# Optimization experiments

Hardware: AMD Instinct MI355X
Metric: run time of the kernel (lower is better)

Reference implementation:

```python
import math
import jax, jax.numpy as jnp
import numpy as np

B, T, E, H = 2, 2048, 1024, 16
HS = E // H  # head size = 64
NEG = jnp.float32(-1e10)


def setup_inputs() -> dict:
    key = jax.random.key(0)
    ks = jax.random.split(key, 7)
    return {
        "query": jax.random.normal(ks[0], (B, T, E), jnp.float32),
        "key": jax.random.normal(ks[1], (B, T, E), jnp.float32),
        "value": jax.random.normal(ks[2], (B, T, E), jnp.float32),
        "Wq": jax.random.normal(ks[3], (E, E), jnp.float32) * 0.02,
        "Wk": jax.random.normal(ks[4], (E, E), jnp.float32) * 0.02,
        "Wv": jax.random.normal(ks[5], (E, E), jnp.float32) * 0.02,
        "Wp": jax.random.normal(ks[6], (E, E), jnp.float32) * 0.02,
    }


def reference(query, key, value, Wq, Wk, Wv, Wp):
    # QKV projections (no bias), split into heads: [B, H, T, HS]
    q = (query @ Wq).reshape(B, T, H, HS).transpose(0, 2, 1, 3)
    k = (key @ Wk).reshape(B, T, H, HS).transpose(0, 2, 1, 3)
    v = (value @ Wv).reshape(B, T, H, HS).transpose(0, 2, 1, 3)
    # scaled dot-product scores [B, H, T, T]
    att = jnp.einsum("bhqd,bhkd->bhqk", q, k) / math.sqrt(HS)
    # additive causal mask (tril allowed)
    causal = jnp.tril(jnp.ones((T, T), dtype=att.dtype))
    att = att + jnp.where(causal == 0, NEG, jnp.float32(0.0))[None, None]
    att = jax.nn.softmax(att, axis=-1)
    # dropout rate 0 / deterministic -> identity
    y = jnp.einsum("bhqk,bhkd->bhqd", att, v)
    y = y.transpose(0, 2, 1, 3).reshape(B, T, E)
    y = y @ Wp
    return y
```

## Files before the change

### kernel.cpp

```cpp
#include <hip/hip_runtime.h>

#define TB 2
#define TT 2048
#define TE 1024
#define TH 16
#define THS 64
#define TM (TB * TT)

typedef __attribute__((ext_vector_type(8))) short short8;
typedef __attribute__((ext_vector_type(4))) float f32x4;
typedef __attribute__((ext_vector_type(16))) float f32x16;

__device__ __forceinline__ f32x4 mfma16(short8 a, short8 b, f32x4 c) {
    return __builtin_amdgcn_mfma_f32_16x16x32_bf16(a, b, c, 0, 0, 0);
}
__device__ __forceinline__ f32x16 mfma32(short8 a, short8 b, f32x16 c) {
    return __builtin_amdgcn_mfma_f32_32x32x16_bf16(a, b, c, 0, 0, 0);
}

__device__ __forceinline__ void gload_lds16(const void* g, void* l) {
    __builtin_amdgcn_global_load_lds(
        (const __attribute__((address_space(1))) void*)g,
        (__attribute__((address_space(3))) void*)l, 16, 0, 0);
}

__device__ __forceinline__ unsigned short f2bf(float f) {
    unsigned int u = __float_as_uint(f);
    u += 0x7fff + ((u >> 16) & 1);
    return (unsigned short)(u >> 16);
}

__device__ __forceinline__ unsigned cvtpk_bf16(float lo, float hi) {
    unsigned r;
    asm("v_cvt_pk_bf16_f32 %0, %1, %2" : "=v"(r) : "v"(lo), "v"(hi));
    return r;
}
__device__ __forceinline__ void plswap(unsigned& a, unsigned& b) {
    asm("v_permlane32_swap_b32 %0, %1" : "+v"(a), "+v"(b));
}

__global__ __launch_bounds__(256) void cast3_f32_bf16(
    const float* __restrict__ a, const float* __restrict__ b,
    const float* __restrict__ c, unsigned short* __restrict__ oa,
    unsigned short* __restrict__ ob, unsigned short* __restrict__ oc, int n4) {
    const float* src = (blockIdx.y == 0) ? a : (blockIdx.y == 1) ? b : c;
    unsigned short* dst = (blockIdx.y == 0) ? oa : (blockIdx.y == 1) ? ob : oc;
    int i = blockIdx.x * 256 + threadIdx.x;
    if (i < n4) {
        float4 v = ((const float4*)src)[i];
        ushort4 o;
        o.x = f2bf(v.x); o.y = f2bf(v.y); o.z = f2bf(v.z); o.w = f2bf(v.w);
        ((ushort4*)dst)[i] = o;
    }
}

__global__ __launch_bounds__(256) void transpose_cast_w4(
    const float* __restrict__ W0, const float* __restrict__ W1,
    const float* __restrict__ W2, const float* __restrict__ W3,
    unsigned short* __restrict__ T0, unsigned short* __restrict__ T1,
    unsigned short* __restrict__ T2, unsigned short* __restrict__ T3) {
    __shared__ float Ts[32][33];
    const int z = blockIdx.z;
    const float* W = (z == 0) ? W0 : (z == 1) ? W1 : (z == 2) ? W2 : W3;
    unsigned short* Wt = (z == 0) ? T0 : (z == 1) ? T1 : (z == 2) ? T2 : T3;
    const int r0 = blockIdx.y * 32, c0 = blockIdx.x * 32;
    const int t = threadIdx.x;
    const int r = t >> 3, c = (t & 7) * 4;
    float4 v = *(const float4*)&W[(size_t)(r0 + r) * TE + c0 + c];
    Ts[r][c] = v.x; Ts[r][c + 1] = v.y; Ts[r][c + 2] = v.z; Ts[r][c + 3] = v.w;
    __syncthreads();
    ushort4 o;
    o.x = f2bf(Ts[c + 0][r]); o.y = f2bf(Ts[c + 1][r]);
    o.z = f2bf(Ts[c + 2][r]); o.w = f2bf(Ts[c + 3][r]);
    *(ushort4*)&Wt[(size_t)(c0 + r) * TE + r0 + c] = o;
}

__global__ __launch_bounds__(512, 2) void gemm_qkv(
    const unsigned short* __restrict__ qc, const unsigned short* __restrict__ kc,
    const unsigned short* __restrict__ vc, const unsigned short* __restrict__ Wqt,
    const unsigned short* __restrict__ Wkt, const unsigned short* __restrict__ Wvt,
    unsigned short* __restrict__ Qb, unsigned short* __restrict__ Kb,
    unsigned short* __restrict__ Vt) {
    __shared__ unsigned short LDS[65536];

    const int z = blockIdx.z;
    const unsigned short* A  = (z == 0) ? qc : (z == 1) ? kc : vc;
    const unsigned short* Bt = (z == 0) ? Wqt : (z == 1) ? Wkt : Wvt;

    const int tid = threadIdx.x;
    const int wv = tid >> 6, lane = tid & 63;
    const int wr = wv >> 2, wc = wv & 3;
    const int quad = lane >> 4, l16 = lane & 15;
    const int bm = blockIdx.x * 256, bn = blockIdx.y * 256;

    const int srow = lane >> 2;
    const int scol = (((lane & 3) ^ ((srow >> 1) & 3))) * 8;
    const int rchunk = (quad ^ ((l16 >> 1) & 3)) * 8;

    f32x4 acc[8][4];
    const f32x4 fz = {0.f, 0.f, 0.f, 0.f};
    #pragma unroll
    for (int i = 0; i < 8; ++i)
        #pragma unroll
        for (int j = 0; j < 4; ++j) acc[i][j] = fz;

    auto stageA = [&](int t, int hi) {
        const int buf = t & 1, k0 = t * 64;
        unsigned short* base = &LDS[buf * 16384];
        #pragma unroll
        for (int j = 0; j < 2; ++j) {
            const int e = wv * 2 + j;
            const int kk = e >> 3, i3 = e & 7;
            const int cr = hi * 4 + (i3 & 3) + ((i3 >> 2) << 3);
            gload_lds16(A + (size_t)(bm + cr * 16 + srow) * TE + k0 + kk * 32 + scol,
                        base + kk * 8192 + cr * 512 + lane * 8);
        }
    };
    auto stageB = [&](int t, int hi) {
        const int buf = t & 1, k0 = t * 64;
        unsigned short* base = &LDS[32768 + buf * 16384];
        #pragma unroll
        for (int j = 0; j < 2; ++j) {
            const int e = wv * 2 + j;
            const int kk = e >> 3, i3 = e & 7;
            const int cc = ((i3 >> 1) << 2) + (i3 & 1) + hi * 2;
            gload_lds16(Bt + (size_t)(bn + cc * 16 + srow) * TE + k0 + kk * 32 + scol,
                        base + kk * 8192 + cc * 512 + lane * 8);
        }
    };

    auto ktile = [&](int t, int buf, bool st, bool predrain) {
        const unsigned short* Al = &LDS[buf * 16384];
        const unsigned short* Bl = &LDS[32768 + buf * 16384];
        short8 af[4][2], blo[2][2], bhi[2][2];
        #pragma unroll
        for (int mi = 0; mi < 4; ++mi)
            #pragma unroll
            for (int kk = 0; kk < 2; ++kk)
                af[mi][kk] = *(const short8*)&Al[kk * 8192 + (wr * 8 + mi) * 512 + l16 * 32 + rchunk];
        #pragma unroll
        for (int nj = 0; nj < 2; ++nj)
            #pragma unroll
            for (int kk = 0; kk < 2; ++kk)
                blo[nj][kk] = *(const short8*)&Bl[kk * 8192 + (wc * 4 + nj) * 512 + l16 * 32 + rchunk];
        __builtin_amdgcn_s_barrier();
        asm volatile("s_waitcnt lgkmcnt(0)" ::: "memory");
        __builtin_amdgcn_sched_barrier(0);
        __builtin_amdgcn_s_setprio(1);
        #pragma unroll
        for (int mi = 0; mi < 4; ++mi)
            #pragma unroll
            for (int nj = 0; nj < 2; ++nj)
                #pragma unroll
                for (int kk = 0; kk < 2; ++kk)
                    acc[mi][nj] = mfma16(af[mi][kk], blo[nj][kk], acc[mi][nj]);
        __builtin_amdgcn_s_setprio(0);
        __builtin_amdgcn_sched_barrier(0);
        __builtin_amdgcn_s_barrier();
        #pragma unroll
        for (int nj = 0; nj < 2; ++nj)
            #pragma unroll
            for (int kk = 0; kk < 2; ++kk)
                bhi[nj][kk] = *(const short8*)&Bl[kk * 8192 + (wc * 4 + 2 + nj) * 512 + l16 * 32 + rchunk];
        if (st) stageA(t + 2, 0);
        __builtin_amdgcn_s_barrier();
        asm volatile("s_waitcnt lgkmcnt(0)" ::: "memory");
        __builtin_amdgcn_sched_barrier(0);
        __builtin_amdgcn_s_setprio(1);
        #pragma unroll
        for (int mi = 0; mi < 4; ++mi)
            #pragma unroll
            for (int nj = 0; nj < 2; ++nj)
                #pragma unroll
                for (int kk = 0; kk < 2; ++kk)
                    acc[mi][2 + nj] = mfma16(af[mi][kk], bhi[nj][kk], acc[mi][2 + nj]);
        __builtin_amdgcn_s_setprio(0);
        __builtin_amdgcn_sched_barrier(0);
        __builtin_amdgcn_s_barrier();
        #pragma unroll
        for (int mi = 0; mi < 4; ++mi)
            #pragma unroll
            for (int kk = 0; kk < 2; ++kk)
                af[mi][kk] = *(const short8*)&Al[kk * 8192 + (wr * 8 + 4 + mi) * 512 + l16 * 32 + rchunk];
        if (st) stageB(t + 2, 0);
        __builtin_amdgcn_s_barrier();
        asm volatile("s_waitcnt lgkmcnt(0)" ::: "memory");
        __builtin_amdgcn_sched_barrier(0);
        __builtin_amdgcn_s_setprio(1);
        #pragma unroll
        for (int mi = 0; mi < 4; ++mi)
            #pragma unroll
            for (int nj = 0; nj < 2; ++nj)
                #pragma unroll
                for (int kk = 0; kk < 2; ++kk)
                    acc[4 + mi][nj] = mfma16(af[mi][kk], blo[nj][kk], acc[4 + mi][nj]);
        __builtin_amdgcn_s_setprio(0);
        __builtin_amdgcn_sched_barrier(0);
        __builtin_amdgcn_s_barrier();
        if (st) { stageB(t + 2, 1); stageA(t + 2, 1); }
        __builtin_amdgcn_s_barrier();
        __builtin_amdgcn_s_setprio(1);
        #pragma unroll
        for (int mi = 0; mi < 4; ++mi)
            #pragma unroll
            for (int nj = 0; nj < 2; ++nj)
                #pragma unroll
                for (int kk = 0; kk < 2; ++kk)
                    acc[4 + mi][2 + nj] = mfma16(af[mi][kk], bhi[nj][kk], acc[4 + mi][2 + nj]);
        __builtin_amdgcn_s_setprio(0);
        __builtin_amdgcn_sched_barrier(0);
        if (st) {
            asm volatile("s_waitcnt vmcnt(8)" ::: "memory");
        } else if (predrain) {
            asm volatile("s_waitcnt vmcnt(0)" ::: "memory");
        }
        __builtin_amdgcn_s_barrier();
    };

    stageA(0, 0); stageB(0, 0); stageB(0, 1); stageA(0, 1);
    stageA(1, 0); stageB(1, 0); stageB(1, 1); stageA(1, 1);
    asm volatile("s_waitcnt vmcnt(8)" ::: "memory");
    __builtin_amdgcn_s_barrier();

    #pragma unroll 1
    for (int t = 0; t < 14; t += 2) {
        ktile(t, 0, true, false);
        ktile(t + 1, 1, true, false);
    }
    ktile(14, 0, false, true);
    ktile(15, 1, false, false);

    if (z < 2) {
        unsigned short* Cb = (z == 0) ? Qb : Kb;
        const float sc = (z == 0) ? 0.18033688011112042f : 1.0f;
        #pragma unroll
        for (int mi = 0; mi < 8; ++mi)
            #pragma unroll
            for (int nj = 0; nj < 4; ++nj) {
                const int m0 = bm + wr * 128 + mi * 16 + quad * 4;
                const int n = bn + wc * 64 + nj * 16 + l16;
                #pragma unroll
                for (int r = 0; r < 4; ++r)
                    Cb[(size_t)(m0 + r) * TE + n] = f2bf(acc[mi][nj][r] * sc);
            }
    } else {
        #pragma unroll
        for (int mi = 0; mi < 8; ++mi)
            #pragma unroll
            for (int nj = 0; nj < 4; ++nj) {
                const int m0 = bm + wr * 128 + mi * 16 + quad * 4;
                const int n = bn + wc * 64 + nj * 16 + l16;
                ushort4 o;
                o.x = f2bf(acc[mi][nj][0]); o.y = f2bf(acc[mi][nj][1]);
                o.z = f2bf(acc[mi][nj][2]); o.w = f2bf(acc[mi][nj][3]);
                size_t idx = ((size_t)((m0 >> 11) * TH + (n >> 6)) * THS + (n & 63)) * TT + (m0 & (TT - 1));
                *(ushort4*)&Vt[idx] = o;
            }
    }
}

__global__ __launch_bounds__(256, 2) void gemm_out(
    const unsigned short* __restrict__ A, const unsigned short* __restrict__ Bt,
    float* __restrict__ C) {
    __shared__ unsigned short As[2][128 * 32];
    __shared__ unsigned short Bs[2][64 * 32];

    const int tid = threadIdx.x;
    const int w = tid >> 6, lane = tid & 63;
    const int quad = lane >> 4, l16 = lane & 15;
    const int bm = blockIdx.x * 128, bn = blockIdx.y * 64;
    const int wm = (w >> 1) * 64, wn = (w & 1) * 32;

    f32x4 acc[4][2];
    const f32x4 fz = {0.f, 0.f, 0.f, 0.f};
    #pragma unroll
    for (int i = 0; i < 4; ++i)
        #pragma unroll
        for (int j = 0; j < 2; ++j) acc[i][j] = fz;

    const int srow = lane >> 2;
    const int scol = (((lane & 3) ^ ((srow >> 1) & 3))) * 8;
    const int rchunk = (quad ^ ((l16 >> 1) & 3)) * 8;

    auto stage = [&](int k0, int buf) {
        #pragma unroll
        for (int i = 0; i < 3; ++i) {
            const int ch = w * 3 + i;
            if (ch < 8)
                gload_lds16(A + (size_t)(bm + ch * 16 + srow) * TE + k0 + scol,
                            &As[buf][ch * 512 + lane * 8]);
            else
                gload_lds16(Bt + (size_t)(bn + (ch - 8) * 16 + srow) * TE + k0 + scol,
                            &Bs[buf][(ch - 8) * 512 + lane * 8]);
        }
    };

    stage(0, 0);
    int cur = 0;
    for (int k0 = 0; k0 < TE; k0 += 32) {
        __syncthreads();
        if (k0 + 32 < TE) stage(k0 + 32, cur ^ 1);

        short8 af[4], bf[2];
        #pragma unroll
        for (int i = 0; i < 4; ++i)
            af[i] = *(const short8*)&As[cur][(wm + i * 16 + l16) * 32 + rchunk];
        #pragma unroll
        for (int j = 0; j < 2; ++j)
            bf[j] = *(const short8*)&Bs[cur][(wn + j * 16 + l16) * 32 + rchunk];
        #pragma unroll
        for (int i = 0; i < 4; ++i)
            #pragma unroll
            for (int j = 0; j < 2; ++j)
                acc[i][j] = mfma16(af[i], bf[j], acc[i][j]);
        cur ^= 1;
    }

    #pragma unroll
    for (int i = 0; i < 4; ++i)
        #pragma unroll
        for (int j = 0; j < 2; ++j) {
            const int m0 = bm + wm + i * 16 + quad * 4;
            const int n = bn + wn + j * 16 + l16;
            #pragma unroll
            for (int r = 0; r < 4; ++r)
                C[(size_t)(m0 + r) * TE + n] = acc[i][j][r];
        }
}

__global__ __launch_bounds__(512, 2) void attn_mfma(
    const unsigned short* __restrict__ Q, const unsigned short* __restrict__ K,
    const unsigned short* __restrict__ Vt, unsigned short* __restrict__ O) {
    __shared__ unsigned short S[49152];
    __shared__ float L0[128];

    const int tid = threadIdx.x;
    const int lane = tid & 63;
    const int wv = tid >> 6;
    const int wk = wv >> 2;
    const int wl = wv & 3;
    const int rl = lane & 31, x = lane >> 5;

    const int lin = blockIdx.x;
    const int bh = lin & 31;
    const int p = lin >> 5;
    const int b = bh >> 4, h = bh & 15;
    const int itA = 15 - p, itB = p;
    const int hA = itA + 1, hB = itB + 1;

    const unsigned short* Kg = K + (size_t)b * TT * TE + h * THS;
    const unsigned short* Vg = Vt + (size_t)bh * THS * TT;

    short8 aqA[4], aqB[4];
    {
        const size_t rA = (size_t)(b * TT + itA * 128 + wl * 32 + rl) * TE + h * THS + x * 8;
        const size_t rB = (size_t)(b * TT + itB * 128 + wl * 32 + rl) * TE + h * THS + x * 8;
        #pragma unroll
        for (int c = 0; c < 4; ++c) {
            aqA[c] = *(const short8*)&Q[rA + c * 16];
            aqB[c] = *(const short8*)&Q[rB + c * 16];
        }
    }

    const int srow = lane >> 2;
    const int scol = (((lane & 3) ^ ((srow >> 1) & 3))) * 8;
    unsigned short* Sg = S + wk * 24576;

    auto stage = [&](int jt, int buf) {
        const int k0 = jt * 64;
        if (wl < 2) {
            #pragma unroll
            for (int j = 0; j < 4; ++j) {
                const int ee = wl * 4 + j;
                const int kk = ee >> 2, r16 = (ee & 3) * 16;
                gload_lds16(Kg + (size_t)(k0 + r16 + srow) * TE + kk * 32 + scol,
                            &Sg[buf * 4096 + ee * 512 + lane * 8]);
            }
        } else {
            #pragma unroll
            for (int j = 0; j < 4; ++j) {
                const int ee = (wl - 2) * 4 + j;
                const int kk = ee >> 2, r16 = (ee & 3) * 16;
                gload_lds16(Vg + (size_t)(r16 + srow) * TT + k0 + kk * 32 + scol,
                            &Sg[12288 + buf * 4096 + ee * 512 + lane * 8]);
            }
        }
    };
    auto stageS = [&](int s) {
        if (s >= 17) return;
        const int it = (s < hA) ? itA : itB;
        const int loc = (s < hA) ? s : s - hA;
        const int jt = (wk ? it + 1 : 0) + loc;
        stage(jt, s % 3);
    };

    stageS(0); stageS(1);

    const int xr = (rl >> 1) & 3;

    auto run_seg = [&](int it, const short8* aq, int sBase, int hSeg) {
        const int q0 = it * 128;
        const int qv = q0 + wl * 32 + rl;
        const int qwMin = q0 + wl * 32;
        f32x16 accO0, accO1;
        #pragma unroll
        for (int i = 0; i < 16; ++i) { accO0[i] = 0.f; accO1[i] = 0.f; }
        float lacc = 0.f;

        for (int i = 0; i < hSeg; ++i) {
            const int s = sBase + i;
            const int buf = s % 3;
            if (s == 16) { asm volatile("s_waitcnt vmcnt(0)" ::: "memory"); }
            else         { asm volatile("s_waitcnt vmcnt(4)" ::: "memory"); }
            __builtin_amdgcn_s_barrier();
            __builtin_amdgcn_sched_barrier(0);
            stageS(s + 2);

            const int jt = (wk ? it + 1 : 0) + i;
            const int k0 = jt * 64;
            const unsigned short* Kb = &Sg[buf * 4096];
            const unsigned short* Vb = &Sg[12288 + buf * 4096];

            f32x16 sa0, sa1;
            #pragma unroll
            for (int i2 = 0; i2 < 16; ++i2) { sa0[i2] = 0.f; sa1[i2] = 0.f; }
            #pragma unroll
            for (int c = 0; c < 4; ++c) {
                const int off = (c >> 1) * 2048 + ((((c & 1) * 2 + x) ^ xr)) * 8;
                short8 kf0 = *(const short8*)&Kb[off + rl * 32];
                short8 kf1 = *(const short8*)&Kb[off + (32 + rl) * 32];
                sa0 = mfma32(kf0, aq[c], sa0);
                sa1 = mfma32(kf1, aq[c], sa1);
            }

            const bool open = (k0 + 63 <= qwMin);
            short8 pb[4];
            #pragma unroll
            for (int mt = 0; mt < 2; ++mt) {
                float pv[16];
                #pragma unroll
                for (int r = 0; r < 16; ++r) {
                    const float sv = (mt == 0) ? sa0[r] : sa1[r];
                    float e = __builtin_amdgcn_exp2f(sv);
                    if (!open) {
                        const int kg = k0 + mt * 32 + (r & 3) + 8 * (r >> 2) + 4 * x;
                        e = (kg > qv) ? 0.f : e;
                    }
                    pv[r] = e;
                    lacc += e;
                }
                unsigned w0 = cvtpk_bf16(pv[0], pv[1]),   w1 = cvtpk_bf16(pv[2], pv[3]);
                unsigned w2 = cvtpk_bf16(pv[4], pv[5]),   w3 = cvtpk_bf16(pv[6], pv[7]);
                unsigned w4 = cvtpk_bf16(pv[8], pv[9]),   w5 = cvtpk_bf16(pv[10], pv[11]);
                unsigned w6 = cvtpk_bf16(pv[12], pv[13]), w7 = cvtpk_bf16(pv[14], pv[15]);
                plswap(w0, w2); plswap(w1, w3);
                plswap(w4, w6); plswap(w5, w7);
                union { unsigned u[4]; short8 s8; } f0, f1;
                f0.u[0] = w0; f0.u[1] = w1; f0.u[2] = w2; f0.u[3] = w3;
                f1.u[0] = w4; f1.u[1] = w5; f1.u[2] = w6; f1.u[3] = w7;
                pb[mt * 2] = f0.s8; pb[mt * 2 + 1] = f1.s8;
            }

            __builtin_amdgcn_s_setprio(1);
            #pragma unroll
            for (int c = 0; c < 4; ++c) {
                const int off = (c >> 1) * 2048 + ((((c & 1) * 2 + x) ^ xr)) * 8;
                short8 vf0 = *(const short8*)&Vb[off + rl * 32];
                short8 vf1 = *(const short8*)&Vb[off + (32 + rl) * 32];
                accO0 = mfma32(vf0, pb[c], accO0);
                accO1 = mfma32(vf1, pb[c], accO1);
            }
            __builtin_amdgcn_s_setprio(0);
        }

        lacc += __shfl_xor(lacc, 32);

        __syncthreads();
        const int lastS = sBase + hSeg - 1;
        const int fb = lastS % 3;
        if (wk == 0) {
            #pragma unroll
            for (int dt = 0; dt < 2; ++dt)
                #pragma unroll
                for (int q4 = 0; q4 < 4; ++q4) {
                    const int i16 = ((dt ^ ((lane >> 2) & 1)) << 4) + ((q4 ^ (lane & 3)) << 2);
                    const int flat = (wl * 64 + lane) * 32 + i16;
                    const int chunk = flat >> 11, offf = flat & 2047;
                    float* dst = (float*)&S[(chunk >> 1) * 24576 + (chunk & 1) * 12288 + fb * 4096] + offf;
                    float4 vstv;
                    if (dt == 0) { vstv.x = accO0[q4*4+0]; vstv.y = accO0[q4*4+1]; vstv.z = accO0[q4*4+2]; vstv.w = accO0[q4*4+3]; }
                    else         { vstv.x = accO1[q4*4+0]; vstv.y = accO1[q4*4+1]; vstv.z = accO1[q4*4+2]; vstv.w = accO1[q4*4+3]; }
                    *(float4*)dst = vstv;
                }
            if (lane < 32) L0[wl * 32 + rl] = lacc;
        }
        __syncthreads();
        if (wk == 1) {
            const float lf = lacc + L0[wl * 32 + rl];
            const float linv = 1.0f / lf;
            unsigned short* Og = O + (size_t)(b * TT + q0 + wl * 32 + rl) * TE + h * THS;
            #pragma unroll
            for (int dt = 0; dt < 2; ++dt)
                #pragma unroll
                for (int q4 = 0; q4 < 4; ++q4) {
                    const int i16 = ((dt ^ ((lane >> 2) & 1)) << 4) + ((q4 ^ (lane & 3)) << 2);
                    const int flat = (wl * 64 + lane) * 32 + i16;
                    const int chunk = flat >> 11, offf = flat & 2047;
                    const float4 vld = *(const float4*)((const float*)&S[(chunk >> 1) * 24576 + (chunk & 1) * 12288 + fb * 4096] + offf);
                    float o0, o1, o2, o3;
                    if (dt == 0) { o0 = accO0[q4*4+0] + vld.x; o1 = accO0[q4*4+1] + vld.y; o2 = accO0[q4*4+2] + vld.z; o3 = accO0[q4*4+3] + vld.w; }
                    else         { o0 = accO1[q4*4+0] + vld.x; o1 = accO1[q4*4+1] + vld.y; o2 = accO1[q4*4+2] + vld.z; o3 = accO1[q4*4+3] + vld.w; }
                    const int dbase = 8 * q4 + 4 * x + 32 * dt;
                    ushort4 o;
                    o.x = f2bf(o0 * linv); o.y = f2bf(o1 * linv);
                    o.z = f2bf(o2 * linv); o.w = f2bf(o3 * linv);
                    *(ushort4*)&Og[dbase] = o;
                }
        }
    };

    run_seg(itA, aqA, 0, hA);
    run_seg(itB, aqB, hA, hB);
}

extern "C" void kernel_launch(void* const* d_in, const int* in_sizes, int n_in,
                              void* d_out, int out_size, void* d_ws, size_t ws_size,
                              hipStream_t stream) {
    const float* q  = (const float*)d_in[0];
    const float* k  = (const float*)d_in[1];
    const float* v  = (const float*)d_in[2];
    const float* Wq = (const float*)d_in[3];
    const float* Wk = (const float*)d_in[4];
    const float* Wv = (const float*)d_in[5];
    const float* Wp = (const float*)d_in[6];
    float* out = (float*)d_out;

    const size_t se = (size_t)TM * TE;
    unsigned short* qc  = (unsigned short*)d_ws;
    unsigned short* kc  = qc + se;
    unsigned short* vc  = kc + se;
    unsigned short* Qb  = vc + se;
    unsigned short* Kb  = Qb + se;
    unsigned short* Vt  = Kb + se;
    unsigned short* Ob  = Vt + se;
    unsigned short* Wqt = Ob + se;
    unsigned short* Wkt = Wqt + (size_t)TE * TE;
    unsigned short* Wvt = Wkt + (size_t)TE * TE;
    unsigned short* Wpt = Wvt + (size_t)TE * TE;

    const int n4 = (int)(se / 4);
    cast3_f32_bf16<<<dim3(n4 / 256, 3), 256, 0, stream>>>(q, k, v, qc, kc, vc, n4);
    transpose_cast_w4<<<dim3(TE / 32, TE / 32, 4), 256, 0, stream>>>(
        Wq, Wk, Wv, Wp, Wqt, Wkt, Wvt, Wpt);

    gemm_qkv<<<dim3(TM / 256, TE / 256, 3), 512, 0, stream>>>(
        qc, kc, vc, Wqt, Wkt, Wvt, Qb, Kb, Vt);

    attn_mfma<<<256, 512, 0, stream>>>(Qb, Kb, Vt, Ob);

    gemm_out<<<dim3(TM / 128, TE / 64), 256, 0, stream>>>(Ob, Wpt, out);
}
```

Before: 204.8 us.

## Shrink QKV GEMM tiles to 128x128 with swizzled grid and fuse prep kernels

```diff
diff --git a/kernel.cpp b/kernel.cpp
--- a/kernel.cpp
+++ b/kernel.cpp
@@ -39,116 +39,118 @@
     asm("v_permlane32_swap_b32 %0, %1" : "+v"(a), "+v"(b));
 }
 
-__global__ __launch_bounds__(256) void cast3_f32_bf16(
-    const float* __restrict__ a, const float* __restrict__ b,
-    const float* __restrict__ c, unsigned short* __restrict__ oa,
-    unsigned short* __restrict__ ob, unsigned short* __restrict__ oc, int n4) {
-    const float* src = (blockIdx.y == 0) ? a : (blockIdx.y == 1) ? b : c;
-    unsigned short* dst = (blockIdx.y == 0) ? oa : (blockIdx.y == 1) ? ob : oc;
-    int i = blockIdx.x * 256 + threadIdx.x;
-    if (i < n4) {
-        float4 v = ((const float4*)src)[i];
-        ushort4 o;
-        o.x = f2bf(v.x); o.y = f2bf(v.y); o.z = f2bf(v.z); o.w = f2bf(v.w);
-        ((ushort4*)dst)[i] = o;
-    }
-}
-
-__global__ __launch_bounds__(256) void transpose_cast_w4(
+__global__ __launch_bounds__(256) void prep(
+    const float* __restrict__ q, const float* __restrict__ k,
+    const float* __restrict__ v, unsigned short* __restrict__ qc,
+    unsigned short* __restrict__ kc, unsigned short* __restrict__ vc,
     const float* __restrict__ W0, const float* __restrict__ W1,
     const float* __restrict__ W2, const float* __restrict__ W3,
     unsigned short* __restrict__ T0, unsigned short* __restrict__ T1,
     unsigned short* __restrict__ T2, unsigned short* __restrict__ T3) {
     __shared__ float Ts[32][33];
-    const int z = blockIdx.z;
-    const float* W = (z == 0) ? W0 : (z == 1) ? W1 : (z == 2) ? W2 : W3;
-    unsigned short* Wt = (z == 0) ? T0 : (z == 1) ? T1 : (z == 2) ? T2 : T3;
-    const int r0 = blockIdx.y * 32, c0 = blockIdx.x * 32;
-    const int t = threadIdx.x;
-    const int r = t >> 3, c = (t & 7) * 4;
-    float4 v = *(const float4*)&W[(size_t)(r0 + r) * TE + c0 + c];
-    Ts[r][c] = v.x; Ts[r][c + 1] = v.y; Ts[r][c + 2] = v.z; Ts[r][c + 3] = v.w;
-    __syncthreads();
-    ushort4 o;
-    o.x = f2bf(Ts[c + 0][r]); o.y = f2bf(Ts[c + 1][r]);
-    o.z = f2bf(Ts[c + 2][r]); o.w = f2bf(Ts[c + 3][r]);
-    *(ushort4*)&Wt[(size_t)(c0 + r) * TE + r0 + c] = o;
-}
-
-__global__ __launch_bounds__(512, 2) void gemm_qkv(
+    const int y = blockIdx.y;
+    if (y < 3) {
+        const float* src = (y == 0) ? q : (y == 1) ? k : v;
+        unsigned short* dst = (y == 0) ? qc : (y == 1) ? kc : vc;
+        const int i = blockIdx.x * 256 + threadIdx.x;
+        float4 vv = ((const float4*)src)[i];
+        ushort4 o;
+        o.x = f2bf(vv.x); o.y = f2bf(vv.y); o.z = f2bf(vv.z); o.w = f2bf(vv.w);
+        ((ushort4*)dst)[i] = o;
+    } else {
+        const int x = blockIdx.x;
+        const int z = x >> 10, rem = x & 1023;
+        const float* W = (z == 0) ? W0 : (z == 1) ? W1 : (z == 2) ? W2 : W3;
+        unsigned short* Wt = (z == 0) ? T0 : (z == 1) ? T1 : (z == 2) ? T2 : T3;
+        const int r0 = ((rem >> 5) & 31) * 32, c0 = (rem & 31) * 32;
+        const int t = threadIdx.x;
+        const int r = t >> 3, c = (t & 7) * 4;
+        float4 vv = *(const float4*)&W[(size_t)(r0 + r) * TE + c0 + c];
+        Ts[r][c] = vv.x; Ts[r][c + 1] = vv.y; Ts[r][c + 2] = vv.z; Ts[r][c + 3] = vv.w;
+        __syncthreads();
+        ushort4 o;
+        o.x = f2bf(Ts[c + 0][r]); o.y = f2bf(Ts[c + 1][r]);
+        o.z = f2bf(Ts[c + 2][r]); o.w = f2bf(Ts[c + 3][r]);
+        *(ushort4*)&Wt[(size_t)(c0 + r) * TE + r0 + c] = o;
+    }
+}
+
+__global__ __launch_bounds__(256, 2) void gemm_qkv(
     const unsigned short* __restrict__ qc, const unsigned short* __restrict__ kc,
     const unsigned short* __restrict__ vc, const unsigned short* __restrict__ Wqt,
     const unsigned short* __restrict__ Wkt, const unsigned short* __restrict__ Wvt,
     unsigned short* __restrict__ Qb, unsigned short* __restrict__ Kb,
     unsigned short* __restrict__ Vt) {
-    __shared__ unsigned short LDS[65536];
-
-    const int z = blockIdx.z;
+    __shared__ unsigned short LDS[32768];
+
+    const int lin = blockIdx.x;
+    const int swz = (lin & 7) * 96 + (lin >> 3);
+    const int z = swz >> 8;
+    const int rem = swz & 255;
+    const int bm = (rem & 31) * 128, bn = (rem >> 5) * 128;
+
     const unsigned short* A  = (z == 0) ? qc : (z == 1) ? kc : vc;
     const unsigned short* Bt = (z == 0) ? Wqt : (z == 1) ? Wkt : Wvt;
 
     const int tid = threadIdx.x;
-    const int wv = tid >> 6, lane = tid & 63;
-    const int wr = wv >> 2, wc = wv & 3;
+    const int w = tid >> 6, lane = tid & 63;
     const int quad = lane >> 4, l16 = lane & 15;
-    const int bm = blockIdx.x * 256, bn = blockIdx.y * 256;
+    const int wm = (w >> 1) * 64, wn = (w & 1) * 64;
 
     const int srow = lane >> 2;
     const int scol = (((lane & 3) ^ ((srow >> 1) & 3))) * 8;
     const int rchunk = (quad ^ ((l16 >> 1) & 3)) * 8;
 
-    f32x4 acc[8][4];
+    f32x4 acc[4][4];
     const f32x4 fz = {0.f, 0.f, 0.f, 0.f};
     #pragma unroll
-    for (int i = 0; i < 8; ++i)
+    for (int i = 0; i < 4; ++i)
         #pragma unroll
         for (int j = 0; j < 4; ++j) acc[i][j] = fz;
 
-    auto stageA = [&](int t, int hi) {
+    auto stageA = [&](int t, int half) {
         const int buf = t & 1, k0 = t * 64;
-        unsigned short* base = &LDS[buf * 16384];
         #pragma unroll
         for (int j = 0; j < 2; ++j) {
-            const int e = wv * 2 + j;
-            const int kk = e >> 3, i3 = e & 7;
-            const int cr = hi * 4 + (i3 & 3) + ((i3 >> 2) << 3);
+            const int e = w * 2 + j;
+            const int kk = e >> 2, i2 = e & 3;
+            const int cr = half * 2 + (i2 & 1) + ((i2 >> 1) << 2);
             gload_lds16(A + (size_t)(bm + cr * 16 + srow) * TE + k0 + kk * 32 + scol,
-                        base + kk * 8192 + cr * 512 + lane * 8);
-        }
-    };
-    auto stageB = [&](int t, int hi) {
+                        &LDS[buf * 8192 + kk * 4096 + cr * 512 + lane * 8]);
+        }
+    };
+    auto stageB = [&](int t, int half) {
         const int buf = t & 1, k0 = t * 64;
-        unsigned short* base = &LDS[32768 + buf * 16384];
         #pragma unroll
         for (int j = 0; j < 2; ++j) {
-            const int e = wv * 2 + j;
-            const int kk = e >> 3, i3 = e & 7;
-            const int cc = ((i3 >> 1) << 2) + (i3 & 1) + hi * 2;
+            const int e = w * 2 + j;
+            const int kk = e >> 2, i2 = e & 3;
+            const int cc = half * 2 + (i2 & 1) + ((i2 >> 1) << 2);
             gload_lds16(Bt + (size_t)(bn + cc * 16 + srow) * TE + k0 + kk * 32 + scol,
-                        base + kk * 8192 + cc * 512 + lane * 8);
-        }
-    };
-
-    auto ktile = [&](int t, int buf, bool st, bool predrain) {
-        const unsigned short* Al = &LDS[buf * 16384];
-        const unsigned short* Bl = &LDS[32768 + buf * 16384];
-        short8 af[4][2], blo[2][2], bhi[2][2];
-        #pragma unroll
-        for (int mi = 0; mi < 4; ++mi)
+                        &LDS[16384 + buf * 8192 + kk * 4096 + cc * 512 + lane * 8]);
+        }
+    };
+
+    auto ktile = [&](int t, bool st, bool last) {
+        const int buf = t & 1;
+        const unsigned short* Al = &LDS[buf * 8192];
+        const unsigned short* Bl = &LDS[16384 + buf * 8192];
+        short8 af[2][2], blo[2][2], bhi[2][2];
+        #pragma unroll
+        for (int mi = 0; mi < 2; ++mi)
             #pragma unroll
             for (int kk = 0; kk < 2; ++kk)
-                af[mi][kk] = *(const short8*)&Al[kk * 8192 + (wr * 8 + mi) * 512 + l16 * 32 + rchunk];
+                af[mi][kk] = *(const short8*)&Al[kk * 4096 + ((w >> 1) * 4 + mi) * 512 + l16 * 32 + rchunk];
         #pragma unroll
         for (int nj = 0; nj < 2; ++nj)
             #pragma unroll
             for (int kk = 0; kk < 2; ++kk)
-                blo[nj][kk] = *(const short8*)&Bl[kk * 8192 + (wc * 4 + nj) * 512 + l16 * 32 + rchunk];
-        __builtin_amdgcn_s_barrier();
+                blo[nj][kk] = *(const short8*)&Bl[kk * 4096 + ((w & 1) * 4 + nj) * 512 + l16 * 32 + rchunk];
         asm volatile("s_waitcnt lgkmcnt(0)" ::: "memory");
         __builtin_amdgcn_sched_barrier(0);
         __builtin_amdgcn_s_setprio(1);
         #pragma unroll
-        for (int mi = 0; mi < 4; ++mi)
+        for (int mi = 0; mi < 2; ++mi)
             #pragma unroll
             for (int nj = 0; nj < 2; ++nj)
                 #pragma unroll
@@ -161,14 +163,13 @@
         for (int nj = 0; nj < 2; ++nj)
             #pragma unroll
             for (int kk = 0; kk < 2; ++kk)
-                bhi[nj][kk] = *(const short8*)&Bl[kk * 8192 + (wc * 4 + 2 + nj) * 512 + l16 * 32 + rchunk];
-        if (st) stageA(t + 2, 0);
-        __builtin_amdgcn_s_barrier();
+                bhi[nj][kk] = *(const short8*)&Bl[kk * 4096 + ((w & 1) * 4 + 2 + nj) * 512 + l16 * 32 + rchunk];
+        if (st) { stageA(t + 2, 0); stageB(t + 2, 0); }
         asm volatile("s_waitcnt lgkmcnt(0)" ::: "memory");
         __builtin_amdgcn_sched_barrier(0);
         __builtin_amdgcn_s_setprio(1);
         #pragma unroll
-        for (int mi = 0; mi < 4; ++mi)
+        for (int mi = 0; mi < 2; ++mi)
             #pragma unroll
             for (int nj = 0; nj < 2; ++nj)
                 #pragma unroll
@@ -178,40 +179,38 @@
         __builtin_amdgcn_sched_barrier(0);
         __builtin_amdgcn_s_barrier();
         #pragma unroll
-        for (int mi = 0; mi < 4; ++mi)
+        for (int mi = 0; mi < 2; ++mi)
             #pragma unroll
             for (int kk = 0; kk < 2; ++kk)
-                af[mi][kk] = *(const short8*)&Al[kk * 8192 + (wr * 8 + 4 + mi) * 512 + l16 * 32 + rchunk];
-        if (st) stageB(t + 2, 0);
+                af[mi][kk] = *(const short8*)&Al[kk * 4096 + ((w >> 1) * 4 + 2 + mi) * 512 + l16 * 32 + rchunk];
+        if (st) stageB(t + 2, 1);
+        asm volatile("s_waitcnt lgkmcnt(0)" ::: "memory");
+        __builtin_amdgcn_sched_barrier(0);
+        __builtin_amdgcn_s_setprio(1);
+        #pragma unroll
+        for (int mi = 0; mi < 2; ++mi)
+            #pragma unroll
+            for (int nj = 0; nj < 2; ++nj)
+                #pragma unroll
+                for (int kk = 0; kk < 2; ++kk)
+                    acc[2 + mi][nj] = mfma16(af[mi][kk], blo[nj][kk], acc[2 + mi][nj]);
+        __builtin_amdgcn_s_setprio(0);
+        __builtin_amdgcn_sched_barrier(0);
         __builtin_amdgcn_s_barrier();
-        asm volatile("s_waitcnt lgkmcnt(0)" ::: "memory");
-        __builtin_amdgcn_sched_barrier(0);
+        if (st) stageA(t + 2, 1);
         __builtin_amdgcn_s_setprio(1);
         #pragma unroll
-        for (int mi = 0; mi < 4; ++mi)
+        for (int mi = 0; mi < 2; ++mi)
             #pragma unroll
             for (int nj = 0; nj < 2; ++nj)
                 #pragma unroll
                 for (int kk = 0; kk < 2; ++kk)
-                    acc[4 + mi][nj] = mfma16(af[mi][kk], blo[nj][kk], acc[4 + mi][nj]);
-        __builtin_amdgcn_s_setprio(0);
-        __builtin_amdgcn_sched_barrier(0);
-        __builtin_amdgcn_s_barrier();
-        if (st) { stageB(t + 2, 1); stageA(t + 2, 1); }
-        __builtin_amdgcn_s_barrier();
-        __builtin_amdgcn_s_setprio(1);
-        #pragma unroll
-        for (int mi = 0; mi < 4; ++mi)
-            #pragma unroll
-            for (int nj = 0; nj < 2; ++nj)
-                #pragma unroll
-                for (int kk = 0; kk < 2; ++kk)
-                    acc[4 + mi][2 + nj] = mfma16(af[mi][kk], bhi[nj][kk], acc[4 + mi][2 + nj]);
+                    acc[2 + mi][2 + nj] = mfma16(af[mi][kk], bhi[nj][kk], acc[2 + mi][2 + nj]);
         __builtin_amdgcn_s_setprio(0);
         __builtin_amdgcn_sched_barrier(0);
         if (st) {
             asm volatile("s_waitcnt vmcnt(8)" ::: "memory");
-        } else if (predrain) {
+        } else if (last) {
             asm volatile("s_waitcnt vmcnt(0)" ::: "memory");
         }
         __builtin_amdgcn_s_barrier();
@@ -223,33 +222,30 @@
     __builtin_amdgcn_s_barrier();
 
     #pragma unroll 1
-    for (int t = 0; t < 14; t += 2) {
-        ktile(t, 0, true, false);
-        ktile(t + 1, 1, true, false);
-    }
-    ktile(14, 0, false, true);
-    ktile(15, 1, false, false);
+    for (int t = 0; t < 14; ++t) ktile(t, true, false);
+    ktile(14, false, true);
+    ktile(15, false, false);
 
     if (z < 2) {
         unsigned short* Cb = (z == 0) ? Qb : Kb;
         const float sc = (z == 0) ? 0.18033688011112042f : 1.0f;
         #pragma unroll
-        for (int mi = 0; mi < 8; ++mi)
+        for (int mi = 0; mi < 4; ++mi)
             #pragma unroll
             for (int nj = 0; nj < 4; ++nj) {
-                const int m0 = bm + wr * 128 + mi * 16 + quad * 4;
-                const int n = bn + wc * 64 + nj * 16 + l16;
+                const int m0 = bm + wm + mi * 16 + quad * 4;
+                const int n = bn + wn + nj * 16 + l16;
                 #pragma unroll
                 for (int r = 0; r < 4; ++r)
                     Cb[(size_t)(m0 + r) * TE + n] = f2bf(acc[mi][nj][r] * sc);
             }
     } else {
         #pragma unroll
-        for (int mi = 0; mi < 8; ++mi)
+        for (int mi = 0; mi < 4; ++mi)
             #pragma unroll
             for (int nj = 0; nj < 4; ++nj) {
-                const int m0 = bm + wr * 128 + mi * 16 + quad * 4;
-                const int n = bn + wc * 64 + nj * 16 + l16;
+                const int m0 = bm + wm + mi * 16 + quad * 4;
+                const int n = bn + wn + nj * 16 + l16;
                 ushort4 o;
                 o.x = f2bf(acc[mi][nj][0]); o.y = f2bf(acc[mi][nj][1]);
                 o.z = f2bf(acc[mi][nj][2]); o.w = f2bf(acc[mi][nj][3]);
@@ -548,13 +544,10 @@
     unsigned short* Wvt = Wkt + (size_t)TE * TE;
     unsigned short* Wpt = Wvt + (size_t)TE * TE;
 
-    const int n4 = (int)(se / 4);
-    cast3_f32_bf16<<<dim3(n4 / 256, 3), 256, 0, stream>>>(q, k, v, qc, kc, vc, n4);
-    transpose_cast_w4<<<dim3(TE / 32, TE / 32, 4), 256, 0, stream>>>(
-        Wq, Wk, Wv, Wp, Wqt, Wkt, Wvt, Wpt);
-
-    gemm_qkv<<<dim3(TM / 256, TE / 256, 3), 512, 0, stream>>>(
-        qc, kc, vc, Wqt, Wkt, Wvt, Qb, Kb, Vt);
+    prep<<<dim3(4096, 4), 256, 0, stream>>>(q, k, v, qc, kc, vc,
+                                            Wq, Wk, Wv, Wp, Wqt, Wkt, Wvt, Wpt);
+
+    gemm_qkv<<<768, 256, 0, stream>>>(qc, kc, vc, Wqt, Wkt, Wvt, Qb, Kb, Vt);
 
     attn_mfma<<<256, 512, 0, stream>>>(Qb, Kb, Vt, Ob);
 
```

New measurement: 206.7 us. No clear change (+0.9%).
